# Optimization experiments

Measured on AMD Instinct MI355X. Metric: run time of the kernel, lower is better.

## Reference

```python
import jax, jax.numpy as jnp
import numpy as np

K = 1024            # atoms per chain
L = 4 * K - 9       # 2*(K-3) sin/cos dihedrals + (K-2) len13 + (K-1) bond lengths
EPS = 1e-6


def _denorm(v, lo, hi):
    # map [-1, 1] -> [lo, hi]
    return (v + 1.0) * 0.5 * (hi - lo) + lo


def _output_arr2values(v):
    # split flat NN output into (sin/cos dihedrals, hedron len13, bond lengths)
    n_d = K - 3
    sc = v[: 2 * n_d].reshape(n_d, 2)                     # (sin, cos) per dihedral
    d13 = _denorm(v[2 * n_d : 2 * n_d + K - 2], 1.5, 5.0)  # 1-3 distances, [1.5, 5]
    bl = _denorm(v[2 * n_d + K - 2 :], 0.9, 3.0)           # bond lengths,  [0.9, 3]
    return sc, d13, bl


def _len2ang(sc, d13, bl):
    # bond angles via law of cosines from consecutive bond lengths + 1-3 distance
    l1, l2 = bl[:-1], bl[1:]
    ct = (l1 * l1 + l2 * l2 - d13 * d13) / (2.0 * l1 * l2)
    theta = jnp.arccos(jnp.clip(ct, -1.0 + EPS, 1.0 - EPS))   # (K-2,) radians
    chi = jnp.arctan2(sc[:, 0], sc[:, 1])                      # (K-3,) radians
    return theta, chi


def _len_ang2coords(bl, theta, chi):
    # sequential NeRF chain extension: place atom i from atoms i-3, i-2, i-1
    a0 = jnp.zeros(3, dtype=bl.dtype)
    a1 = jnp.array([1.0, 0.0, 0.0], dtype=bl.dtype) * bl[0]
    t0 = theta[0]
    a2 = a1 + bl[1] * jnp.stack([-jnp.cos(t0), jnp.sin(t0), jnp.zeros((), bl.dtype)])

    def step(carry, inp):
        a, b, c = carry
        l, th, ch = inp
        bc = c - b
        bc = bc / (jnp.linalg.norm(bc) + EPS)
        n = jnp.cross(b - a, bc)
        n = n / (jnp.linalg.norm(n) + EPS)
        m = jnp.cross(n, bc)
        st = jnp.sin(th)
        d = c + l * (-jnp.cos(th) * bc + st * jnp.cos(ch) * m + st * jnp.sin(ch) * n)
        return (b, c, d), d

    _, rest = jax.lax.scan(step, (a0, a1, a2), (bl[2:], theta[1:], chi))
    return jnp.concatenate([jnp.stack([a0, a1, a2]), rest], axis=0)  # (K, 3)


def _chain2coords(v):
    sc, d13, bl = _output_arr2values(v)
    theta, chi = _len2ang(sc, d13, bl)
    return _len_ang2coords(bl, theta, chi)


def setup_inputs() -> dict:
    key = jax.random.key(0)
    k1, k2 = jax.random.split(key)
    B = 2048
    predictions = 2.0 * jax.random.uniform(k1, (B, L), dtype=jnp.float32) - 1.0
    targets = 2.0 * jax.random.uniform(k2, (B, L), dtype=jnp.float32) - 1.0
    return {"predictions": predictions, "targets": targets}


def reference(predictions, targets):
    p = jnp.clip(predictions, -1.0, 1.0)           # only predictions are clamped
    pred_coords = jax.vmap(_chain2coords)(p)        # (B, K, 3)
    targ_coords = jax.vmap(_chain2coords)(targets)  # (B, K, 3)
    return jnp.mean(jnp.square(pred_coords - targ_coords))
```

## Files before the change

### kernel.cpp

```cpp
#include <hip/hip_runtime.h>


#define LROW  4087
#define NSTEP 1021
#define NROW  2048
#define CHUNK 8
#define EPSF  1e-6f
#define INVMEAN (1.0f / (2048.0f * 1024.0f * 3.0f))

__device__ __forceinline__ float frcp(float x){ return __builtin_amdgcn_rcpf(x); }
__device__ __forceinline__ float frsq(float x){ return __builtin_amdgcn_rsqf(x); }

__global__ void __launch_bounds__(256, 4)
rmsd_kernel(const float* __restrict__ pred, const float* __restrict__ targ,
            float* __restrict__ ws){
  __shared__ float pos[128*25 + 8];
  __shared__ float Tbuf[2][12];
  __shared__ float ini[3];
  __shared__ float part;

  const int row  = blockIdx.x;
  const int tid  = threadIdx.x;
  const int ln   = tid & 63;
  const int wv   = tid >> 6;
  const int c    = wv >> 1;
  const int half = wv & 1;
  const int lid  = (half << 6) | ln;
  const int j0   = lid * CHUNK;

  const float* __restrict__ v = (c ? targ : pred) + (size_t)row * LROW;
  const float cl = c ? 1e30f : 1.0f;

  const float rb0 = fminf(fmaxf(v[3064], -cl), cl);
  const float rd0 = fminf(fmaxf(v[2042], -cl), cl);
  const float rb1w= fminf(fmaxf(v[3065], -cl), cl);

  float s0[CHUNK], s1[CHUNK], dd[CHUNK], bv[CHUNK+1];
  #pragma unroll
  for (int k = 0; k < CHUNK; ++k){
    s0[k] = v[2*(j0+k)];
    s1[k] = v[2*(j0+k)+1];
    dd[k] = v[2043 + j0 + k];
  }
  #pragma unroll
  for (int m = 0; m <= CHUNK; ++m){
    int ix = 3065 + j0 + m;
    if (ix > 4086) ix = 4086;
    bv[m] = v[ix];
  }
  #pragma unroll
  for (int m = 0; m <= CHUNK; ++m)
    bv[m] = fmaf(fminf(fmaxf(bv[m], -cl), cl), 1.05f, 1.95f);

  float c0x,c0y,c0z, c1x,c1y,c1z, c2x,c2y,c2z, tx,ty,tz;
  float tl[CHUNK][3];
  #pragma unroll
  for (int k = 0; k < CHUNK; ++k){
    const float a0 = fminf(fmaxf(s0[k], -cl), cl);
    const float a1 = fminf(fmaxf(s1[k], -cl), cl);
    const float d  = fmaf(fminf(fmaxf(dd[k], -cl), cl), 1.75f, 3.25f);
    const float b1 = bv[k], b2 = bv[k+1];
    float ct = (b1*b1 + b2*b2 - d*d) * frcp(2.0f*b1*b2);
    ct = fminf(fmaxf(ct, -1.0f + EPSF), 1.0f - EPSF);
    const float omc = fmaxf(1.0f - ct*ct, 1e-12f);
    const float ist = frsq(omc);
    const float st  = omc * ist;
    const float r2 = a0*a0 + a1*a1;
    const bool ok = r2 > 1e-36f;
    const float ir = ok ? frsq(r2) : 0.0f;
    const float scv = a0 * ir;
    const float ccv = ok ? a1 * ir : 1.0f;
    const float hx = -ct, hy = st*ccv, hz = st*scv;
    if (k == 0){
      c0x=hx;      c0y=hy;      c0z=hz;
      c1x=-st;     c1y=hx*ccv;  c1z=hx*scv;
      c2x=0.0f;    c2y=-scv;    c2z=ccv;
      tx=b2*hx;    ty=b2*hy;    tz=b2*hz;
    } else {
      const float n0x = c0x*hx + c1x*hy + c2x*hz;
      const float n0y = c0y*hx + c1y*hy + c2y*hz;
      const float n0z = c0z*hx + c1z*hy + c2z*hz;
      tx = fmaf(b2, n0x, tx); ty = fmaf(b2, n0y, ty); tz = fmaf(b2, n0z, tz);
      const float n1x = ist * fmaf(hx, n0x, -c0x);
      const float n1y = ist * fmaf(hx, n0y, -c0y);
      const float n1z = ist * fmaf(hx, n0z, -c0z);
      const float n2x = fmaf(ccv, c2x, -scv*c1x);
      const float n2y = fmaf(ccv, c2y, -scv*c1y);
      const float n2z = fmaf(ccv, c2z, -scv*c1z);
      c0x=n0x; c0y=n0y; c0z=n0z;
      c1x=n1x; c1y=n1y; c1z=n1z;
      c2x=n2x; c2y=n2y; c2z=n2z;
    }
    tl[k][0]=tx; tl[k][1]=ty; tl[k][2]=tz;
  }

  float r0x=c0x, r0y=c0y, r0z=c0z, r1x=c1x, r1y=c1y, r1z=c1z;
  #pragma unroll
  for (int off = 1; off < 64; off <<= 1){
    const float o0x=__shfl_up(r0x,off), o0y=__shfl_up(r0y,off), o0z=__shfl_up(r0z,off);
    const float o1x=__shfl_up(r1x,off), o1y=__shfl_up(r1y,off), o1z=__shfl_up(r1z,off);
    const float o2x = o0y*o1z - o0z*o1y;
    const float o2y = o0z*o1x - o0x*o1z;
    const float o2z = o0x*o1y - o0y*o1x;
    const float n0x = o0x*r0x + o1x*r0y + o2x*r0z;
    const float n0y = o0y*r0x + o1y*r0y + o2y*r0z;
    const float n0z = o0z*r0x + o1z*r0y + o2z*r0z;
    const float n1x = o0x*r1x + o1x*r1y + o2x*r1z;
    const float n1y = o0y*r1x + o1y*r1y + o2y*r1z;
    const float n1z = o0z*r1x + o1z*r1y + o2z*r1z;
    if (ln >= off){
      r0x=n0x; r0y=n0y; r0z=n0z;
      r1x=n1x; r1y=n1y; r1z=n1z;
    }
  }

  float e0x=__shfl_up(r0x,1), e0y=__shfl_up(r0y,1), e0z=__shfl_up(r0z,1);
  float e1x=__shfl_up(r1x,1), e1y=__shfl_up(r1y,1), e1z=__shfl_up(r1z,1);
  if (ln == 0){ e0x=1.f; e0y=0.f; e0z=0.f; e1x=0.f; e1y=1.f; e1z=0.f; }

  {
    const float x2x = e0y*e1z - e0z*e1y;
    const float x2y = e0z*e1x - e0x*e1z;
    const float x2z = e0x*e1y - e0y*e1x;
    const float wx = e0x*tx + e1x*ty + x2x*tz;
    const float wy = e0y*tx + e1y*ty + x2y*tz;
    const float wz = e0z*tx + e1z*ty + x2z*tz;
    float sx=wx, sy=wy, sz=wz;
    #pragma unroll
    for (int off = 1; off < 64; off <<= 1){
      const float ax=__shfl_up(sx,off), ay=__shfl_up(sy,off), az=__shfl_up(sz,off);
      if (ln >= off){ sx+=ax; sy+=ay; sz+=az; }
    }
    tx = sx - wx; ty = sy - wy; tz = sz - wz;

    if (half == 0 && ln == 63){
      Tbuf[c][0]=r0x; Tbuf[c][1]=r0y; Tbuf[c][2]=r0z;
      Tbuf[c][3]=r1x; Tbuf[c][4]=r1y; Tbuf[c][5]=r1z;
      Tbuf[c][6]=sx;  Tbuf[c][7]=sy;  Tbuf[c][8]=sz;
    }
  }
  __syncthreads();

  if (half == 1){
    const float T0x=Tbuf[c][0], T0y=Tbuf[c][1], T0z=Tbuf[c][2];
    const float T1x=Tbuf[c][3], T1y=Tbuf[c][4], T1z=Tbuf[c][5];
    const float T2x = T0y*T1z - T0z*T1y;
    const float T2y = T0z*T1x - T0x*T1z;
    const float T2z = T0x*T1y - T0y*T1x;
    const float f0x = T0x*e0x + T1x*e0y + T2x*e0z;
    const float f0y = T0y*e0x + T1y*e0y + T2y*e0z;
    const float f0z = T0z*e0x + T1z*e0y + T2z*e0z;
    const float f1x = T0x*e1x + T1x*e1y + T2x*e1z;
    const float f1y = T0y*e1x + T1y*e1y + T2y*e1z;
    const float f1z = T0z*e1x + T1z*e1y + T2z*e1z;
    const float ntx = Tbuf[c][6] + T0x*tx + T1x*ty + T2x*tz;
    const float nty = Tbuf[c][7] + T0y*tx + T1y*ty + T2y*tz;
    const float ntz = Tbuf[c][8] + T0z*tx + T1z*ty + T2z*tz;
    e0x=f0x; e0y=f0y; e0z=f0z; e1x=f1x; e1y=f1y; e1z=f1z;
    tx=ntx; ty=nty; tz=ntz;
  }

  const float bl0 = fmaf(rb0,  1.05f, 1.95f);
  const float d0  = fmaf(rd0,  1.75f, 3.25f);
  const float b1f = fmaf(rb1w, 1.05f, 1.95f);
  float ct0 = (bl0*bl0 + b1f*b1f - d0*d0) * frcp(2.0f*bl0*b1f);
  ct0 = fminf(fmaxf(ct0, -1.0f + EPSF), 1.0f - EPSF);
  const float st0 = sqrtf(fmaxf(1.0f - ct0*ct0, 0.0f));
  const float a1x = bl0;
  const float a2x = bl0 - b1f*ct0;
  const float a2y = b1f*st0;

  const float e2x = e0y*e1z - e0z*e1y;
  const float e2y = e0z*e1x - e0x*e1z;
  const float e2z = e0x*e1y - e0y*e1x;

  const float g0x = -ct0*e0x - st0*e0y, g0y = st0*e0x - ct0*e0y, g0z = e0z;
  const float g1x = -ct0*e1x - st0*e1y, g1y = st0*e1x - ct0*e1y, g1z = e1z;
  const float g2x = -ct0*e2x - st0*e2y, g2y = st0*e2x - ct0*e2y, g2z = e2z;
  const float gtx = a2x - ct0*tx - st0*ty;
  const float gty = a2y + st0*tx - ct0*ty;
  const float gtz = tz;

  #pragma unroll
  for (int k = 0; k < CHUNK; ++k){
    const float ux = tl[k][0], uy = tl[k][1], uz = tl[k][2];
    tl[k][0] = gtx + g0x*ux + g1x*uy + g2x*uz;
    tl[k][1] = gty + g0y*ux + g1y*uy + g2y*uz;
    tl[k][2] = gtz + g0z*ux + g1z*uy + g2z*uz;
  }

  if (c == 0){
    #pragma unroll
    for (int k = 0; k < CHUNK; ++k){
      if (j0 + k < NSTEP){
        const int o = lid*25 + 3*k;
        pos[o] = tl[k][0]; pos[o+1] = tl[k][1]; pos[o+2] = tl[k][2];
      }
    }
    if (lid == 0){ ini[0] = a1x; ini[1] = a2x; ini[2] = a2y; }
  }
  __syncthreads();

  float acc = 0.0f;
  if (c == 1){
    if (lid == 0){
      const float dx = ini[0] - a1x;
      const float dy = ini[1] - a2x;
      const float dz = ini[2] - a2y;
      acc = dx*dx + dy*dy + dz*dz;
    }
    #pragma unroll
    for (int k = 0; k < CHUNK; ++k){
      if (j0 + k < NSTEP){
        const int o = lid*25 + 3*k;
        const float dx = pos[o]   - tl[k][0];
        const float dy = pos[o+1] - tl[k][1];
        const float dz = pos[o+2] - tl[k][2];
        acc = fmaf(dx, dx, acc);
        acc = fmaf(dy, dy, acc);
        acc = fmaf(dz, dz, acc);
      }
    }
    #pragma unroll
    for (int off = 32; off > 0; off >>= 1) acc += __shfl_down(acc, off);
    if (half == 1 && ln == 0) part = acc;
  }
  __syncthreads();
  if (wv == 2 && ln == 0) ws[row] = acc + part;
}

__global__ void __launch_bounds__(256, 1)
reduce_kernel(const float* __restrict__ ws, float* __restrict__ out){
  __shared__ float wsum[4];
  const int tid = threadIdx.x;
  float a = 0.0f;
  #pragma unroll
  for (int i = 0; i < 8; ++i) a += ws[tid + (i << 8)];
  #pragma unroll
  for (int off = 32; off > 0; off >>= 1) a += __shfl_down(a, off);
  if ((tid & 63) == 0) wsum[tid >> 6] = a;
  __syncthreads();
  if (tid == 0) out[0] = (wsum[0] + wsum[1] + wsum[2] + wsum[3]) * INVMEAN;
}

extern "C" void kernel_launch(void* const* d_in, const int* in_sizes, int n_in,
                              void* d_out, int out_size, void* d_ws, size_t ws_size,
                              hipStream_t stream) {
  const float* pred = (const float*)d_in[0];
  const float* targ = (const float*)d_in[1];
  float* out = (float*)d_out;
  float* ws  = (float*)d_ws;

  rmsd_kernel<<<NROW, 256, 0, stream>>>(pred, targ, ws);
  reduce_kernel<<<1, 256, 0, stream>>>(ws, out);
}
```

Measured before the change: 102.1 us.

## Process each chain with one wave using 16-step chunks instead of two waves

Each chain (pred or targ) is now handled by a single 64-lane wave that composes 16 NeRF steps per lane, instead of two waves with 8 steps each. This removes the cross-wave transform hand-off through shared memory, one block barrier and the final partial-sum exchange, and halves the block size to 128 threads. In exchange each lane does twice the serial local composition and holds more registers, and there are half as many waves per row to hide latency.

```diff
diff --git a/kernel.cpp b/kernel.cpp
--- a/kernel.cpp
+++ b/kernel.cpp
@@ -4,32 +4,27 @@
 #define LROW  4087
 #define NSTEP 1021
 #define NROW  2048
-#define CHUNK 8
+#define CHUNK 16
 #define EPSF  1e-6f
 #define INVMEAN (1.0f / (2048.0f * 1024.0f * 3.0f))
 
 __device__ __forceinline__ float frcp(float x){ return __builtin_amdgcn_rcpf(x); }
 __device__ __forceinline__ float frsq(float x){ return __builtin_amdgcn_rsqf(x); }
 
-__global__ void __launch_bounds__(256, 4)
+__global__ void __launch_bounds__(128) __attribute__((amdgpu_waves_per_eu(4, 4)))
 rmsd_kernel(const float* __restrict__ pred, const float* __restrict__ targ,
             float* __restrict__ ws){
-  __shared__ float pos[128*25 + 8];
-  __shared__ float Tbuf[2][12];
+  __shared__ float pos[64*49 + 48 + 2];
   __shared__ float ini[3];
-  __shared__ float part;
 
   const int row  = blockIdx.x;
   const int tid  = threadIdx.x;
   const int ln   = tid & 63;
   const int wv   = tid >> 6;
-  const int c    = wv >> 1;
-  const int half = wv & 1;
-  const int lid  = (half << 6) | ln;
-  const int j0   = lid * CHUNK;
-
-  const float* __restrict__ v = (c ? targ : pred) + (size_t)row * LROW;
-  const float cl = c ? 1e30f : 1.0f;
+  const int j0   = ln * CHUNK;
+
+  const float* __restrict__ v = (wv ? targ : pred) + (size_t)row * LROW;
+  const float cl = wv ? 1e30f : 1.0f;
 
   const float rb0 = fminf(fmaxf(v[3064], -cl), cl);
   const float rd0 = fminf(fmaxf(v[2042], -cl), cl);
@@ -132,32 +127,6 @@
       if (ln >= off){ sx+=ax; sy+=ay; sz+=az; }
     }
     tx = sx - wx; ty = sy - wy; tz = sz - wz;
-
-    if (half == 0 && ln == 63){
-      Tbuf[c][0]=r0x; Tbuf[c][1]=r0y; Tbuf[c][2]=r0z;
-      Tbuf[c][3]=r1x; Tbuf[c][4]=r1y; Tbuf[c][5]=r1z;
-      Tbuf[c][6]=sx;  Tbuf[c][7]=sy;  Tbuf[c][8]=sz;
-    }
-  }
-  __syncthreads();
-
-  if (half == 1){
-    const float T0x=Tbuf[c][0], T0y=Tbuf[c][1], T0z=Tbuf[c][2];
-    const float T1x=Tbuf[c][3], T1y=Tbuf[c][4], T1z=Tbuf[c][5];
-    const float T2x = T0y*T1z - T0z*T1y;
-    const float T2y = T0z*T1x - T0x*T1z;
-    const float T2z = T0x*T1y - T0y*T1x;
-    const float f0x = T0x*e0x + T1x*e0y + T2x*e0z;
-    const float f0y = T0y*e0x + T1y*e0y + T2y*e0z;
-    const float f0z = T0z*e0x + T1z*e0y + T2z*e0z;
-    const float f1x = T0x*e1x + T1x*e1y + T2x*e1z;
-    const float f1y = T0y*e1x + T1y*e1y + T2y*e1z;
-    const float f1z = T0z*e1x + T1z*e1y + T2z*e1z;
-    const float ntx = Tbuf[c][6] + T0x*tx + T1x*ty + T2x*tz;
-    const float nty = Tbuf[c][7] + T0y*tx + T1y*ty + T2y*tz;
-    const float ntz = Tbuf[c][8] + T0z*tx + T1z*ty + T2z*tz;
-    e0x=f0x; e0y=f0y; e0z=f0z; e1x=f1x; e1y=f1y; e1z=f1z;
-    tx=ntx; ty=nty; tz=ntz;
   }
 
   const float bl0 = fmaf(rb0,  1.05f, 1.95f);
@@ -189,21 +158,21 @@
     tl[k][2] = gtz + g0z*ux + g1z*uy + g2z*uz;
   }
 
-  if (c == 0){
+  if (wv == 0){
     #pragma unroll
     for (int k = 0; k < CHUNK; ++k){
       if (j0 + k < NSTEP){
-        const int o = lid*25 + 3*k;
+        const int o = ln*49 + 3*k;
         pos[o] = tl[k][0]; pos[o+1] = tl[k][1]; pos[o+2] = tl[k][2];
       }
     }
-    if (lid == 0){ ini[0] = a1x; ini[1] = a2x; ini[2] = a2y; }
+    if (ln == 0){ ini[0] = a1x; ini[1] = a2x; ini[2] = a2y; }
   }
   __syncthreads();
 
-  float acc = 0.0f;
-  if (c == 1){
-    if (lid == 0){
+  if (wv == 1){
+    float acc = 0.0f;
+    if (ln == 0){
       const float dx = ini[0] - a1x;
       const float dy = ini[1] - a2x;
       const float dz = ini[2] - a2y;
@@ -212,7 +181,7 @@
     #pragma unroll
     for (int k = 0; k < CHUNK; ++k){
       if (j0 + k < NSTEP){
-        const int o = lid*25 + 3*k;
+        const int o = ln*49 + 3*k;
         const float dx = pos[o]   - tl[k][0];
         const float dy = pos[o+1] - tl[k][1];
         const float dz = pos[o+2] - tl[k][2];
@@ -223,10 +192,8 @@
     }
     #pragma unroll
     for (int off = 32; off > 0; off >>= 1) acc += __shfl_down(acc, off);
-    if (half == 1 && ln == 0) part = acc;
-  }
-  __syncthreads();
-  if (wv == 2 && ln == 0) ws[row] = acc + part;
+    if (ln == 0) ws[row] = acc;
+  }
 }
 
 __global__ void __launch_bounds__(256, 1)
@@ -251,6 +218,6 @@
   float* out = (float*)d_out;
   float* ws  = (float*)d_ws;
 
-  rmsd_kernel<<<NROW, 256, 0, stream>>>(pred, targ, ws);
+  rmsd_kernel<<<NROW, 128, 0, stream>>>(pred, targ, ws);
   reduce_kernel<<<1, 256, 0, stream>>>(ws, out);
 }
```

Result: faster. 96.73 us (-5.3%).
